# Performance work log

Measured on AMD Instinct MI355X. Metric: run time of the kernel, lower is better.

## Reference

```python
import jax, jax.numpy as jnp
import numpy as np

N_NODES = 50000
N_EDGES = 800000
IN_F, H_F, OUT_F = 256, 256, 128


def setup_inputs() -> dict:
    key = jax.random.key(0)
    k1, k2, k3, k4, k5, k6 = jax.random.split(key, 6)
    in_feat = jax.random.normal(k1, (N_NODES, IN_F), dtype=jnp.float32)
    src = jax.random.randint(k2, (N_EDGES,), 0, N_NODES, dtype=jnp.int32)
    dst = jax.random.randint(k3, (N_EDGES,), 0, N_NODES, dtype=jnp.int32)
    s1 = 1.0 / np.sqrt(IN_F)
    s2 = 1.0 / np.sqrt(H_F)
    W1 = jax.random.uniform(k4, (IN_F, H_F), dtype=jnp.float32, minval=-s1, maxval=s1)
    b1 = jnp.zeros((H_F,), dtype=jnp.float32)
    W2 = jax.random.uniform(k5, (H_F, OUT_F), dtype=jnp.float32, minval=-s2, maxval=s2)
    b2 = jnp.zeros((OUT_F,), dtype=jnp.float32)
    return {"in_feat": in_feat, "src": src, "dst": dst,
            "W1": W1, "b1": b1, "W2": W2, "b2": b2}


def _graph_conv(x, W, b, src, dst, n_nodes):
    # DGL GraphConv with norm='both':
    #   h = D_in^{-1/2} A D_out^{-1/2} (X W) + b   (degrees clamped to min 1)
    ones = jnp.ones((src.shape[0],), dtype=x.dtype)
    deg_out = jax.ops.segment_sum(ones, src, num_segments=n_nodes)
    deg_in = jax.ops.segment_sum(ones, dst, num_segments=n_nodes)
    norm_out = jax.lax.rsqrt(jnp.maximum(deg_out, 1.0))  # [N]
    norm_in = jax.lax.rsqrt(jnp.maximum(deg_in, 1.0))    # [N]
    h = (x @ W) * norm_out[:, None]                       # [N, F_out]
    agg = jax.ops.segment_sum(h[src], dst, num_segments=n_nodes)  # SpMM
    return agg * norm_in[:, None] + b


def reference(in_feat, src, dst, W1, b1, W2, b2):
    n = in_feat.shape[0]
    h = _graph_conv(in_feat, W1, b1, src, dst, n)
    h = jax.nn.relu(h)
    h = _graph_conv(h, W2, b2, src, dst, n)
    # dgl.mean_nodes over a single graph -> mean across all nodes
    return jnp.mean(h, axis=0)  # [OUT_F]
```

## Files before the change

kernel.cpp:

```cpp
#include <hip/hip_runtime.h>


#define NNODES 50000
#define NEDGES 800000
#define G1_BM   ((NNODES + 127) / 128)
#define MEGA_NB 3911
#define WS_NB   2048
#define NQUAD   (NNODES / 4)

typedef __bf16 bf16x8 __attribute__((ext_vector_type(8)));
typedef float f32x4 __attribute__((ext_vector_type(4)));
typedef float f32x2 __attribute__((ext_vector_type(2)));

__device__ __forceinline__ unsigned short f2b(float f) {
    union { float f; unsigned u; } v; v.f = f;
    unsigned r = 0x7fffu + ((v.u >> 16) & 1u);
    return (unsigned short)((v.u + r) >> 16);
}
__device__ __forceinline__ unsigned char f2fp8(float x) {
    return (unsigned char)(__builtin_amdgcn_cvt_pk_fp8_f32(x, x, 0, false) & 0xff);
}
__device__ __forceinline__ float rdeg(int d) {
    return __frsqrt_rn((float)max(d, 1));
}

__global__ void k_cast_w1(const float* __restrict__ W1, unsigned short* __restrict__ W1t,
                          int* __restrict__ deg0) {
    int id = blockIdx.x * blockDim.x + threadIdx.x;
    int k = id >> 8, n = id & 255;
    W1t[n * 256 + k] = f2b(W1[id]);
    deg0[id] = 0;
    int j = id + 65536;
    if (j < 2 * NNODES) deg0[j] = 0;
}

__global__ __launch_bounds__(256) void k_mega1(
    const int* __restrict__ src, const int* __restrict__ dst,
    int* __restrict__ degOut, int* __restrict__ degIn,
    unsigned short* __restrict__ col2, unsigned short* __restrict__ dst2,
    const float* __restrict__ X, const unsigned short* __restrict__ W1t,
    unsigned char* __restrict__ H, int M) {
    __shared__ __align__(16) unsigned short As[128][40];
    __shared__ __align__(16) unsigned short Bs[128][40];

    int bid = blockIdx.x;
    int tid = threadIdx.x;

    if ((bid % 5) != 4) {
        int did = bid - (bid + 1) / 5;
        int e = did * 256 + tid;
        if (e < NEDGES) {
            int s = src[e], d = dst[e];
            int si = atomicAdd(&degIn[d], 1);
            if (si < 64) col2[d * 64 + si] = (unsigned short)s;
            int so = atomicAdd(&degOut[s], 1);
            if (so < 64) dst2[s * 64 + so] = (unsigned short)d;
        }
        return;
    }

    int g = bid / 5;
    int bm = g % G1_BM, bn = g / G1_BM;
    int m0 = bm * 128, n0 = bn * 128;
    int lane = tid & 63, wave = tid >> 6;
    int wm = (wave >> 1) * 64, wn = (wave & 1) * 64;
    int q = lane >> 4, r16 = lane & 15;

    f32x4 acc[4][4];
#pragma unroll
    for (int i = 0; i < 4; i++)
#pragma unroll
        for (int j = 0; j < 4; j++) acc[i][j] = 0.f;

    int c0 = tid, c1 = tid + 256;
    int r0 = c0 >> 2, k0c = (c0 & 3) * 8;
    int r1 = c1 >> 2, k1c = (c1 & 3) * 8;
    const float* Ar0 = X + (size_t)min(m0 + r0, M - 1) * 256;
    const float* Ar1 = X + (size_t)min(m0 + r1, M - 1) * 256;
    const unsigned short* Br0 = W1t + (size_t)(n0 + r0) * 256;
    const unsigned short* Br1 = W1t + (size_t)(n0 + r1) * 256;

    auto pk2u = [](float a, float b) -> unsigned {
        unsigned short x = f2b(a), y = f2b(b);
        return (unsigned)x | ((unsigned)y << 16);
    };

    for (int k0 = 0; k0 < 256; k0 += 32) {
        float4 fa0 = *(const float4*)(Ar0 + k0 + k0c);
        float4 fa1 = *(const float4*)(Ar0 + k0 + k0c + 4);
        float4 fb0 = *(const float4*)(Ar1 + k0 + k1c);
        float4 fb1 = *(const float4*)(Ar1 + k0 + k1c + 4);
        uint4 vb0 = *(const uint4*)(Br0 + k0 + k0c);
        uint4 vb1 = *(const uint4*)(Br1 + k0 + k1c);
        uint4 va0 = make_uint4(pk2u(fa0.x, fa0.y), pk2u(fa0.z, fa0.w), pk2u(fa1.x, fa1.y), pk2u(fa1.z, fa1.w));
        uint4 va1 = make_uint4(pk2u(fb0.x, fb0.y), pk2u(fb0.z, fb0.w), pk2u(fb1.x, fb1.y), pk2u(fb1.z, fb1.w));
        __syncthreads();
        *(uint4*)&As[r0][k0c] = va0;
        *(uint4*)&As[r1][k1c] = va1;
        *(uint4*)&Bs[r0][k0c] = vb0;
        *(uint4*)&Bs[r1][k1c] = vb1;
        __syncthreads();
        bf16x8 af[4], bf[4];
#pragma unroll
        for (int i = 0; i < 4; i++)
            af[i] = *(const bf16x8*)&As[wm + i * 16 + r16][q * 8];
#pragma unroll
        for (int j = 0; j < 4; j++)
            bf[j] = *(const bf16x8*)&Bs[wn + j * 16 + r16][q * 8];
#pragma unroll
        for (int i = 0; i < 4; i++)
#pragma unroll
            for (int j = 0; j < 4; j++)
                acc[i][j] = __builtin_amdgcn_mfma_f32_16x16x32_bf16(af[i], bf[j], acc[i][j], 0, 0, 0);
    }

#pragma unroll
    for (int i = 0; i < 4; i++) {
#pragma unroll
        for (int rr = 0; rr < 4; rr++) {
            int m = m0 + wm + i * 16 + q * 4 + rr;
            if (m < M) {
                unsigned char* Hp = H + (size_t)m * 256 + n0 + wn + r16;
#pragma unroll
                for (int j = 0; j < 4; j++)
                    Hp[j * 16] = f2fp8(acc[i][j][rr]);
            }
        }
    }
}

__global__ __launch_bounds__(256) void k_spmm_wsum(
    const unsigned char* __restrict__ H, const int* __restrict__ degIn,
    const int* __restrict__ degOut, const unsigned short* __restrict__ col2,
    const unsigned short* __restrict__ dst2, const float* __restrict__ bias,
    float* __restrict__ vpart) {
    __shared__ float sm[4][256];
    int wave = threadIdx.x >> 6;
    int lane = threadIdx.x & 63;
    int f = lane * 4;
    const unsigned char* Hf = H + f;
    float4 bv = *(const float4*)(bias + f);
    float vac0 = 0.f, vac1 = 0.f, vac2 = 0.f, vac3 = 0.f;

    int qd = blockIdx.x;
    int node = qd * 4 + wave;
    int pDI = 0, pDO = 0, pc = 0, pd = 0;
    if (qd < NQUAD) {
        pDI = degIn[node]; pDO = degOut[node];
        pc = (int)col2[(size_t)node * 64 + lane];
        pd = (int)dst2[(size_t)node * 64 + lane];
    }

    while (qd < NQUAD) {
        int dI = min(pDI, 64), dO = min(pDO, 64);
        int myc = pc, myd = pd;

        int nqd = qd + gridDim.x;
        if (nqd < NQUAD) {
            int nn = nqd * 4 + wave;
            pDI = degIn[nn]; pDO = degOut[nn];
            pc = (int)col2[(size_t)nn * 64 + lane];
            pd = (int)dst2[(size_t)nn * 64 + lane];
        }

        float sIn = 0.f;
        if (lane < dO) sIn = rdeg(degIn[myd]);
#pragma unroll
        for (int o = 32; o > 0; o >>= 1) sIn += __shfl_xor(sIn, o);
        float wn = rdeg(dO) * sIn;

        float a0 = 0.f, a1 = 0.f, a2 = 0.f, a3 = 0.f;
        int i = 0;
        for (; i + 16 <= dI; i += 16) {
            float w[16]; unsigned v[16];
#pragma unroll
            for (int u = 0; u < 16; u++) {
                int c = __builtin_amdgcn_readlane(myc, i + u);
                w[u] = rdeg(degOut[c]);
                v[u] = *(const unsigned*)(Hf + (size_t)c * 256);
            }
#pragma unroll
            for (int u = 0; u < 16; u++) {
                f32x2 lo = __builtin_amdgcn_cvt_pk_f32_fp8(v[u], false);
                f32x2 hi = __builtin_amdgcn_cvt_pk_f32_fp8(v[u], true);
                a0 += lo.x * w[u]; a1 += lo.y * w[u];
                a2 += hi.x * w[u]; a3 += hi.y * w[u];
            }
        }
        for (; i + 4 <= dI; i += 4) {
            float w[4]; unsigned v[4];
#pragma unroll
            for (int u = 0; u < 4; u++) {
                int c = __builtin_amdgcn_readlane(myc, i + u);
                w[u] = rdeg(degOut[c]);
                v[u] = *(const unsigned*)(Hf + (size_t)c * 256);
            }
#pragma unroll
            for (int u = 0; u < 4; u++) {
                f32x2 lo = __builtin_amdgcn_cvt_pk_f32_fp8(v[u], false);
                f32x2 hi = __builtin_amdgcn_cvt_pk_f32_fp8(v[u], true);
                a0 += lo.x * w[u]; a1 += lo.y * w[u];
                a2 += hi.x * w[u]; a3 += hi.y * w[u];
            }
        }
        for (; i < dI; i++) {
            int c = __builtin_amdgcn_readlane(myc, i);
            float w = rdeg(degOut[c]);
            unsigned v = *(const unsigned*)(Hf + (size_t)c * 256);
            f32x2 lo = __builtin_amdgcn_cvt_pk_f32_fp8(v, false);
            f32x2 hi = __builtin_amdgcn_cvt_pk_f32_fp8(v, true);
            a0 += lo.x * w; a1 += lo.y * w;
            a2 += hi.x * w; a3 += hi.y * w;
        }

        float nm = rdeg(dI);
        vac0 += wn * fmaxf(a0 * nm + bv.x, 0.f);
        vac1 += wn * fmaxf(a1 * nm + bv.y, 0.f);
        vac2 += wn * fmaxf(a2 * nm + bv.z, 0.f);
        vac3 += wn * fmaxf(a3 * nm + bv.w, 0.f);

        qd = nqd;
    }

    *(float4*)&sm[wave][f] = make_float4(vac0, vac1, vac2, vac3);
    __syncthreads();
    int t = threadIdx.x;
    float s4 = sm[0][t] + sm[1][t] + sm[2][t] + sm[3][t];
    vpart[(size_t)blockIdx.x * 256 + t] = s4;
}

__global__ __launch_bounds__(256) void k_red1(const float* __restrict__ vpart,
                                              float* __restrict__ vred) {
    int b = blockIdx.x;
    int t = threadIdx.x;
    float s = 0.f;
    for (int i = b; i < WS_NB; i += 64) s += vpart[(size_t)i * 256 + t];
    vred[(size_t)b * 256 + t] = s;
}

__global__ __launch_bounds__(1024) void k_final(
    const float* __restrict__ vred, const float* __restrict__ W2,
    const float* __restrict__ b2, float* __restrict__ out) {
    __shared__ float part[4][256];
    __shared__ float v[256];
    int t = threadIdx.x;
    int feat = t & 255, pr = t >> 8;
    float s = 0.f;
    for (int i = pr; i < 64; i += 4) s += vred[(size_t)i * 256 + feat];
    part[pr][feat] = s;
    __syncthreads();
    if (t < 256) v[t] = part[0][t] + part[1][t] + part[2][t] + part[3][t];
    __syncthreads();
    if (t < 128) {
        float o = 0.f;
        for (int k = 0; k < 256; k++) o += v[k] * W2[k * 128 + t];
        out[t] = o * (1.0f / (float)NNODES) + b2[t];
    }
}

extern "C" void kernel_launch(void* const* d_in, const int* in_sizes, int n_in,
                              void* d_out, int out_size, void* d_ws, size_t ws_size,
                              hipStream_t stream) {
    const float* X   = (const float*)d_in[0];
    const int*   src = (const int*)d_in[1];
    const int*   dst = (const int*)d_in[2];
    const float* W1  = (const float*)d_in[3];
    const float* b1  = (const float*)d_in[4];
    const float* W2  = (const float*)d_in[5];
    const float* b2  = (const float*)d_in[6];
    float* out = (float*)d_out;

    const int n = NNODES;

    char* p = (char*)d_ws;
    auto carve = [&](size_t bytes) -> void* {
        void* r = (void*)p;
        p += (bytes + 255) & ~(size_t)255;
        return r;
    };
    int*   degOut  = (int*)carve((size_t)2 * n * sizeof(int));
    int*   degIn   = degOut + n;
    unsigned short* col2 = (unsigned short*)carve((size_t)n * 64 * 2);
    unsigned short* dst2 = (unsigned short*)carve((size_t)n * 64 * 2);
    unsigned short* W1t  = (unsigned short*)carve((size_t)256 * 256 * 2);
    unsigned char*  bufA = (unsigned char*)carve((size_t)n * 256);
    float* vpart  = (float*)carve((size_t)WS_NB * 256 * sizeof(float));
    float* vred   = (float*)carve((size_t)64 * 256 * sizeof(float));

    k_cast_w1<<<256, 256, 0, stream>>>(W1, W1t, degOut);

    k_mega1<<<MEGA_NB, 256, 0, stream>>>(src, dst, degOut, degIn, col2, dst2, X, W1t, bufA, n);

    k_spmm_wsum<<<WS_NB, 256, 0, stream>>>(bufA, degIn, degOut, col2, dst2, b1, vpart);

    k_red1<<<64, 256, 0, stream>>>(vpart, vred);
    k_final<<<1, 1024, 0, stream>>>(vred, W2, b2, out);
}
```

Baseline: 223.3 us.

## Pad degree counters to separate cache lines and precompute normalization arrays

```diff
diff --git a/kernel.cpp b/kernel.cpp
--- a/kernel.cpp
+++ b/kernel.cpp
@@ -3,6 +3,7 @@
 
 #define NNODES 50000
 #define NEDGES 800000
+#define DPAD   32
 #define G1_BM   ((NNODES + 127) / 128)
 #define MEGA_NB 3911
 #define WS_NB   2048
@@ -25,13 +26,12 @@
 }
 
 __global__ void k_cast_w1(const float* __restrict__ W1, unsigned short* __restrict__ W1t,
-                          int* __restrict__ deg0) {
+                          uint4* __restrict__ deg0) {
     int id = blockIdx.x * blockDim.x + threadIdx.x;
     int k = id >> 8, n = id & 255;
     W1t[n * 256 + k] = f2b(W1[id]);
-    deg0[id] = 0;
-    int j = id + 65536;
-    if (j < 2 * NNODES) deg0[j] = 0;
+    const uint4 z = make_uint4(0, 0, 0, 0);
+    for (int j = id; j < 2 * NNODES * DPAD / 4; j += 65536) deg0[j] = z;
 }
 
 __global__ __launch_bounds__(256) void k_mega1(
@@ -51,9 +51,9 @@
         int e = did * 256 + tid;
         if (e < NEDGES) {
             int s = src[e], d = dst[e];
-            int si = atomicAdd(&degIn[d], 1);
+            int si = atomicAdd(&degIn[d * DPAD], 1);
             if (si < 64) col2[d * 64 + si] = (unsigned short)s;
-            int so = atomicAdd(&degOut[s], 1);
+            int so = atomicAdd(&degOut[s * DPAD], 1);
             if (so < 64) dst2[s * 64 + so] = (unsigned short)d;
         }
         return;
@@ -129,11 +129,24 @@
     }
 }
 
+__global__ __launch_bounds__(256) void k_norms(
+    const int* __restrict__ degOut, const int* __restrict__ degIn,
+    float* __restrict__ normOut, float* __restrict__ normIn,
+    int* __restrict__ degc) {
+    int i = blockIdx.x * blockDim.x + threadIdx.x;
+    if (i < NNODES) {
+        int dI = degIn[i * DPAD], dO = degOut[i * DPAD];
+        normIn[i] = rdeg(dI);
+        normOut[i] = rdeg(dO);
+        degc[i] = min(dI, 64) | (min(dO, 64) << 16);
+    }
+}
+
 __global__ __launch_bounds__(256) void k_spmm_wsum(
-    const unsigned char* __restrict__ H, const int* __restrict__ degIn,
-    const int* __restrict__ degOut, const unsigned short* __restrict__ col2,
-    const unsigned short* __restrict__ dst2, const float* __restrict__ bias,
-    float* __restrict__ vpart) {
+    const unsigned char* __restrict__ H, const float* __restrict__ normIn,
+    const float* __restrict__ normOut, const int* __restrict__ degc,
+    const unsigned short* __restrict__ col2, const unsigned short* __restrict__ dst2,
+    const float* __restrict__ bias, float* __restrict__ vpart) {
     __shared__ float sm[4][256];
     int wave = threadIdx.x >> 6;
     int lane = threadIdx.x & 63;
@@ -144,30 +157,32 @@
 
     int qd = blockIdx.x;
     int node = qd * 4 + wave;
-    int pDI = 0, pDO = 0, pc = 0, pd = 0;
+    int pDC = 0, pc = 0, pd = 0;
+    float pNI = 0.f, pNO = 0.f;
     if (qd < NQUAD) {
-        pDI = degIn[node]; pDO = degOut[node];
+        pDC = degc[node]; pNI = normIn[node]; pNO = normOut[node];
         pc = (int)col2[(size_t)node * 64 + lane];
         pd = (int)dst2[(size_t)node * 64 + lane];
     }
 
     while (qd < NQUAD) {
-        int dI = min(pDI, 64), dO = min(pDO, 64);
+        int dI = pDC & 0xffff, dO = pDC >> 16;
+        float nI = pNI, nO = pNO;
         int myc = pc, myd = pd;
 
         int nqd = qd + gridDim.x;
         if (nqd < NQUAD) {
             int nn = nqd * 4 + wave;
-            pDI = degIn[nn]; pDO = degOut[nn];
+            pDC = degc[nn]; pNI = normIn[nn]; pNO = normOut[nn];
             pc = (int)col2[(size_t)nn * 64 + lane];
             pd = (int)dst2[(size_t)nn * 64 + lane];
         }
 
         float sIn = 0.f;
-        if (lane < dO) sIn = rdeg(degIn[myd]);
+        if (lane < dO) sIn = normIn[myd];
 #pragma unroll
         for (int o = 32; o > 0; o >>= 1) sIn += __shfl_xor(sIn, o);
-        float wn = rdeg(dO) * sIn;
+        float wn = nO * sIn;
 
         float a0 = 0.f, a1 = 0.f, a2 = 0.f, a3 = 0.f;
         int i = 0;
@@ -176,7 +191,7 @@
 #pragma unroll
             for (int u = 0; u < 16; u++) {
                 int c = __builtin_amdgcn_readlane(myc, i + u);
-                w[u] = rdeg(degOut[c]);
+                w[u] = normOut[c];
                 v[u] = *(const unsigned*)(Hf + (size_t)c * 256);
             }
 #pragma unroll
@@ -192,7 +207,7 @@
 #pragma unroll
             for (int u = 0; u < 4; u++) {
                 int c = __builtin_amdgcn_readlane(myc, i + u);
-                w[u] = rdeg(degOut[c]);
+                w[u] = normOut[c];
                 v[u] = *(const unsigned*)(Hf + (size_t)c * 256);
             }
 #pragma unroll
@@ -205,7 +220,7 @@
         }
         for (; i < dI; i++) {
             int c = __builtin_amdgcn_readlane(myc, i);
-            float w = rdeg(degOut[c]);
+            float w = normOut[c];
             unsigned v = *(const unsigned*)(Hf + (size_t)c * 256);
             f32x2 lo = __builtin_amdgcn_cvt_pk_f32_fp8(v, false);
             f32x2 hi = __builtin_amdgcn_cvt_pk_f32_fp8(v, true);
@@ -213,11 +228,10 @@
             a2 += hi.x * w; a3 += hi.y * w;
         }
 
-        float nm = rdeg(dI);
-        vac0 += wn * fmaxf(a0 * nm + bv.x, 0.f);
-        vac1 += wn * fmaxf(a1 * nm + bv.y, 0.f);
-        vac2 += wn * fmaxf(a2 * nm + bv.z, 0.f);
-        vac3 += wn * fmaxf(a3 * nm + bv.w, 0.f);
+        vac0 += wn * fmaxf(a0 * nI + bv.x, 0.f);
+        vac1 += wn * fmaxf(a1 * nI + bv.y, 0.f);
+        vac2 += wn * fmaxf(a2 * nI + bv.z, 0.f);
+        vac3 += wn * fmaxf(a3 * nI + bv.w, 0.f);
 
         qd = nqd;
     }
@@ -278,20 +292,25 @@
         p += (bytes + 255) & ~(size_t)255;
         return r;
     };
-    int*   degOut  = (int*)carve((size_t)2 * n * sizeof(int));
-    int*   degIn   = degOut + n;
+    int*   degOut  = (int*)carve((size_t)2 * n * DPAD * sizeof(int));
+    int*   degIn   = degOut + (size_t)n * DPAD;
     unsigned short* col2 = (unsigned short*)carve((size_t)n * 64 * 2);
     unsigned short* dst2 = (unsigned short*)carve((size_t)n * 64 * 2);
     unsigned short* W1t  = (unsigned short*)carve((size_t)256 * 256 * 2);
     unsigned char*  bufA = (unsigned char*)carve((size_t)n * 256);
     float* vpart  = (float*)carve((size_t)WS_NB * 256 * sizeof(float));
     float* vred   = (float*)carve((size_t)64 * 256 * sizeof(float));
-
-    k_cast_w1<<<256, 256, 0, stream>>>(W1, W1t, degOut);
+    float* normOutD = (float*)carve((size_t)n * sizeof(float));
+    float* normInD  = (float*)carve((size_t)n * sizeof(float));
+    int*   degc     = (int*)carve((size_t)n * sizeof(int));
+
+    k_cast_w1<<<256, 256, 0, stream>>>(W1, W1t, (uint4*)degOut);
 
     k_mega1<<<MEGA_NB, 256, 0, stream>>>(src, dst, degOut, degIn, col2, dst2, X, W1t, bufA, n);
 
-    k_spmm_wsum<<<WS_NB, 256, 0, stream>>>(bufA, degIn, degOut, col2, dst2, b1, vpart);
+    k_norms<<<(n + 255) / 256, 256, 0, stream>>>(degOut, degIn, normOutD, normInD, degc);
+
+    k_spmm_wsum<<<WS_NB, 256, 0, stream>>>(bufA, normInD, normOutD, degc, col2, dst2, b1, vpart);
 
     k_red1<<<64, 256, 0, stream>>>(vpart, vred);
     k_final<<<1, 1024, 0, stream>>>(vred, W2, b2, out);
```

New measurement: 230.2 us. +3.1%, slower.
